# Kernel tuning notes

Hardware: AMD Instinct MI355X
Metric: run time of the kernel (lower is better)

## Reference

```python
import jax, jax.numpy as jnp
import numpy as np

COMMA_ID = 1010   # BERT wordpiece id for ','
H, NH, HD = 768, 8, 96
B, S = 64, 512
NSEG = 17         # 16 commas per row -> 17 segments
EPS = 1e-5


def setup_inputs() -> dict:
    key = jax.random.key(0)
    ks = jax.random.split(key, 16)
    text_hs = jax.random.normal(ks[0], (B, S, H), jnp.float32)
    cols_hs = jax.random.normal(ks[1], (B, S, H), jnp.float32)
    ids = jax.random.randint(ks[2], (B, S), 0, 30522)
    ids = jnp.where(ids == COMMA_ID, COMMA_ID + 1, ids)  # avoid accidental commas
    comma_pos = jnp.arange(16, 257, 16)                  # 16 commas per row
    ids = ids.at[:, comma_pos].set(COMMA_ID)
    sc = 0.02
    wq = jax.random.normal(ks[3], (H, H), jnp.float32) * sc
    wk = jax.random.normal(ks[4], (H, H), jnp.float32) * sc
    wv = jax.random.normal(ks[5], (H, H), jnp.float32) * sc
    bq = jnp.zeros((H,), jnp.float32)
    bk = jnp.zeros((H,), jnp.float32)
    bv = jnp.zeros((H,), jnp.float32)
    wo = jax.random.normal(ks[6], (H, H), jnp.float32) * sc
    bo = jnp.zeros((H,), jnp.float32)
    gamma = jnp.ones((H,), jnp.float32)
    beta = jnp.zeros((H,), jnp.float32)
    w_out = jax.random.normal(ks[7], (1, H), jnp.float32) * sc
    b_out = jnp.zeros((1,), jnp.float32)
    return dict(text_hs=text_hs, cols_hs=cols_hs, wq=wq, wk=wk, wv=wv,
                bq=bq, bk=bk, bv=bv, wo=wo, bo=bo, gamma=gamma, beta=beta,
                w_out=w_out, b_out=b_out, columns_input_ids=ids, n_segments=NSEG)


def _forward(text_hs, cols_hs, wq, wk, wv, bq, bk, bv, wo, bo,
             gamma, beta, w_out, b_out, columns_input_ids, n_segments):
    t = text_hs[:, 1:, :]   # drop first token, as in forward()  [B, L, H]
    c = cols_hs[:, 1:, :]
    L = t.shape[1]
    # --- nn.MultiheadAttention(query=cols, key=value=text), batch_first ---
    q = c @ wq.T + bq
    k = t @ wk.T + bk
    v = t @ wv.T + bv
    split = lambda x: x.reshape(x.shape[0], -1, NH, HD).transpose(0, 2, 1, 3)
    scores = jnp.einsum('bhqd,bhkd->bhqk', split(q), split(k)) / np.sqrt(HD).astype(np.float32)
    attn = jax.nn.softmax(scores, axis=-1)
    ctx = jnp.einsum('bhqk,bhkd->bhqd', attn, split(v))
    ctx = ctx.transpose(0, 2, 1, 3).reshape(c.shape[0], L, H)
    attn_out = ctx @ wo.T + bo
    # --- BatchNorm1d over channels (training-mode batch stats) ---
    xt = attn_out.transpose(0, 2, 1)            # [B, H, L]
    mu = xt.mean(axis=(0, 2), keepdims=True)
    var = xt.var(axis=(0, 2), keepdims=True)     # biased, as torch BN normalization
    xn = (xt - mu) / jnp.sqrt(var + EPS) * gamma[None, :, None] + beta[None, :, None]
    cross_out = c + xn.transpose(0, 2, 1)       # residual add
    fv = (cross_out @ w_out.T + b_out).squeeze(-1)   # [B, L] scores per token
    # --- compose_outputs: mean-pool comma-delimited ragged spans ---
    is_comma = columns_input_ids[:, :L] == COMMA_ID
    seg = jnp.cumsum(is_comma.astype(jnp.int32), axis=1) - is_comma.astype(jnp.int32)
    mask = (jnp.arange(L)[None, :] >= 1) & (~is_comma)    # slice_start=1, commas excluded
    oh = ((seg[:, :, None] == jnp.arange(n_segments)[None, None, :])
          & mask[:, :, None]).astype(fv.dtype)            # [B, L, J]
    sums = jnp.einsum('blj,bl->bj', oh, fv)
    cnt = oh.sum(axis=1)
    return sums / jnp.maximum(cnt, 1.0)                   # [B, n_segments]


def reference(text_hs, cols_hs, wq, wk, wv, bq, bk, bv, wo, bo,
              gamma, beta, w_out, b_out, columns_input_ids, n_segments):
    return _forward(text_hs, cols_hs, wq, wk, wv, bq, bk, bv, wo, bo,
                    gamma, beta, w_out, b_out, columns_input_ids, n_segments)
```

## Files before the change

### kernel.cpp

```cpp
#include <hip/hip_runtime.h>
#include <hip/hip_bf16.h>

#define COMMA_IDC 1010
#define NHEAD 8
#define Ll 511
#define Mrows 32704
#define NSEG 17

typedef __attribute__((ext_vector_type(8))) short bf16x8;
typedef __attribute__((ext_vector_type(4))) float f32x4;
typedef unsigned short u16;
typedef unsigned int u32;
typedef unsigned long long u64;

__device__ __forceinline__ u16 f2b(float f) {
  __hip_bfloat16 h = __float2bfloat16(f);
  return *reinterpret_cast<u16*>(&h);
}
__device__ __forceinline__ float b2f(u16 u) {
  u32 x = ((u32)u) << 16;
  return __builtin_bit_cast(float, x);
}

__device__ __forceinline__ void gld_lds16(const void* g, void* l) {
  __builtin_amdgcn_global_load_lds(
      (const __attribute__((address_space(1))) void*)(u64)g,
      (__attribute__((address_space(3))) void*)(u32)(u64)l,
      16, 0, 0);
}

#define MFMA16(a, b, c) __builtin_amdgcn_mfma_f32_16x16x32_bf16(a, b, c, 0, 0, 0)
#define LGKM0 do { asm volatile("s_waitcnt lgkmcnt(0)" ::: "memory"); __builtin_amdgcn_sched_barrier(0); } while (0)

__global__ void conv_w(const float4* __restrict__ wq, const float4* __restrict__ wk,
                       const float4* __restrict__ wv, const float4* __restrict__ wo,
                       ushort4* __restrict__ wqkvb, ushort4* __restrict__ wob) {
  int i = blockIdx.x * 256 + threadIdx.x;
  int seg = i / 147456, off = i - seg * 147456;
  const float4* s = (seg == 0) ? wq : ((seg == 1) ? wk : ((seg == 2) ? wv : wo));
  ushort4* d = (seg == 3) ? wob : (wqkvb + seg * 147456);
  float4 v = s[off];
  ushort4 o; o.x = f2b(v.x); o.y = f2b(v.y); o.z = f2b(v.z); o.w = f2b(v.w);
  d[off] = o;
}

__global__ void zero_kernel(float* p, int n) {
  int i = blockIdx.x * 256 + threadIdx.x;
  if (i < n) p[i] = 0.f;
}

#define LDA(db, i, kk) (*(const bf16x8*)(sMem + (db) + wr * 8192 + ((i) * 16 + fr) * 64 + ((((kk) * 4 + fq) ^ xm) << 3)))
#define LDW(db, j, kk) (*(const bf16x8*)(sMem + (db) + 16384 + (((wc * 64 + (j) * 16) >> 7) * 8192) + \
                     (((wc * 64 + (j) * 16) & 127) + fr) * 64 + ((((kk) * 4 + fq) ^ xm) << 3)))

template<int NTILES, int NOUT, int QNT, bool AF32, bool DO_STATS>
__global__ __launch_bounds__(512, 2) void gemm256(
    const void* __restrict__ A0v, const void* __restrict__ A1v, const u16* __restrict__ W,
    const float* __restrict__ b0, const float* __restrict__ b1, const float* __restrict__ b2,
    u16* __restrict__ outp, float* __restrict__ ssum, float* __restrict__ ssq)
{
  __shared__ __align__(16) u16 sMem[65536];
  const int tid = threadIdx.x;
  const int lane = tid & 63, wid = tid >> 6;
  const int fr = lane & 15, fq = lane >> 4;
  const int wr = wid >> 2, wc = wid & 3;
  const int xm = fr & 7;

  int fid = blockIdx.x;
  int xcd = fid & 7, w = fid >> 3;
  int mrow = xcd * 16 + w / NTILES;
  int ncol = w - (w / NTILES) * NTILES;
  const int m0 = mrow * 256, n0 = ncol * 256;

  const int rS = tid >> 3;
  const int cS = (tid & 7) ^ (rS & 7);
  const u16* gW0 = W + (u64)(n0 + rS) * 768 + cS * 8;
  const u16* gW1 = W + (u64)(n0 + 128 + rS) * 768 + cS * 8;
  const u32 st0 = tid * 8;

  const float* fA = (ncol < QNT) ? (const float*)A0v : (const float*)A1v;
  const u16*   uA = (ncol < QNT) ? (const u16*)A0v : (const u16*)A1v;
  const float* aSrc[4];
  u32 aDst[4];
  if constexpr (AF32) {
#pragma unroll
    for (int c4 = 0; c4 < 4; c4++) {
      int c = tid + c4 * 512;
      int half = c >> 10, rowin = (c >> 3) & 127, p = c & 7;
      int m = m0 + half * 128 + rowin;
      if (m > Mrows - 1) m = Mrows - 1;
      int srcrow = m + m / 511 + 1;
      int s = p ^ (rowin & 7);
      aSrc[c4] = fA + (u64)srcrow * 768 + s * 8;
      aDst[c4] = (u32)(half * 8192 + rowin * 64 + p * 8);
    }
  }
  const u16* gA0u = nullptr;
  const u16* gA1u = nullptr;
  if constexpr (!AF32) {
    gA0u = uA + (u64)(m0 + rS) * 768 + cS * 8;
    gA1u = uA + (u64)(m0 + 128 + rS) * 768 + cS * 8;
  }

  f32x4 acc[8][4] = {};
  bf16x8 af[4][2], wf[4][2];
  float4 rA[8];

  auto stageW = [&](int buf, int kt) {
    const int kb = kt * 64;
    const u32 db = (u32)buf * 32768 + 16384;
    gld_lds16(gW0 + kb, sMem + db + st0);
    gld_lds16(gW0 + kb + 49152, sMem + db + st0 + 4096);
    gld_lds16(gW1 + kb, sMem + db + 8192 + st0);
    gld_lds16(gW1 + kb + 49152, sMem + db + 8192 + st0 + 4096);
  };
  auto stageAu = [&](int buf, int kt) {
    const int kb = kt * 64;
    const u32 db = (u32)buf * 32768;
    gld_lds16(gA0u + kb, sMem + db + st0);
    gld_lds16(gA0u + kb + 49152, sMem + db + st0 + 4096);
    gld_lds16(gA1u + kb, sMem + db + 8192 + st0);
    gld_lds16(gA1u + kb + 49152, sMem + db + 8192 + st0 + 4096);
  };
  auto loadA = [&](int kt) {
#pragma unroll
    for (int c4 = 0; c4 < 4; c4++) {
      rA[2 * c4]     = *(const float4*)(aSrc[c4] + kt * 64);
      rA[2 * c4 + 1] = *(const float4*)(aSrc[c4] + kt * 64 + 4);
    }
  };
  auto writeA = [&](int buf) {
    const u32 db = (u32)buf * 32768;
#pragma unroll
    for (int c4 = 0; c4 < 4; c4++) {
      const float4 x = rA[2 * c4], y = rA[2 * c4 + 1];
      bf16x8 v;
      v[0] = (short)f2b(x.x); v[1] = (short)f2b(x.y); v[2] = (short)f2b(x.z); v[3] = (short)f2b(x.w);
      v[4] = (short)f2b(y.x); v[5] = (short)f2b(y.y); v[6] = (short)f2b(y.z); v[7] = (short)f2b(y.w);
      *(bf16x8*)(sMem + db + aDst[c4]) = v;
    }
  };

  if constexpr (AF32) {
    stageW(0, 0);
    loadA(0);
    writeA(0);
    loadA(1);
  } else {
    stageAu(0, 0);
    stageW(0, 0);
    asm volatile("s_waitcnt vmcnt(0)" ::: "memory");
  }
  LGKM0;
  __builtin_amdgcn_s_barrier();

  for (int kt = 0; kt < 12; ++kt) {
    const u32 db = (u32)(kt & 1) * 32768;
#pragma unroll
    for (int i = 0; i < 4; i++) { af[i][0] = LDA(db, i, 0); af[i][1] = LDA(db, i, 1); }
#pragma unroll
    for (int j = 0; j < 4; j++) { wf[j][0] = LDW(db, j, 0); wf[j][1] = LDW(db, j, 1); }
    if (kt + 1 < 12) {
      if constexpr (AF32) {
        writeA((kt + 1) & 1);
        stageW((kt + 1) & 1, kt + 1);
        if (kt + 2 < 12) loadA(kt + 2);
      } else {
        stageAu((kt + 1) & 1, kt + 1);
        stageW((kt + 1) & 1, kt + 1);
      }
    }
    __builtin_amdgcn_s_barrier();
    LGKM0;
    __builtin_amdgcn_s_setprio(1);
#pragma unroll
    for (int i = 0; i < 4; i++)
#pragma unroll
      for (int j = 0; j < 4; j++) {
        acc[i][j] = MFMA16(af[i][0], wf[j][0], acc[i][j]);
        acc[i][j] = MFMA16(af[i][1], wf[j][1], acc[i][j]);
      }
    __builtin_amdgcn_s_setprio(0);
    __builtin_amdgcn_s_barrier();
#pragma unroll
    for (int i = 0; i < 4; i++) { af[i][0] = LDA(db, i + 4, 0); af[i][1] = LDA(db, i + 4, 1); }
    LGKM0;
    __builtin_amdgcn_s_setprio(1);
#pragma unroll
    for (int i = 0; i < 4; i++)
#pragma unroll
      for (int j = 0; j < 4; j++) {
        acc[i + 4][j] = MFMA16(af[i][0], wf[j][0], acc[i + 4][j]);
        acc[i + 4][j] = MFMA16(af[i][1], wf[j][1], acc[i + 4][j]);
      }
    __builtin_amdgcn_s_setprio(0);
    if (kt + 1 < 12) {
      if constexpr (AF32) {
        if (kt + 2 < 12) { asm volatile("s_waitcnt vmcnt(8)" ::: "memory"); }
        else             { asm volatile("s_waitcnt vmcnt(0)" ::: "memory"); }
      } else {
        asm volatile("s_waitcnt vmcnt(0)" ::: "memory");
      }
    }
    __builtin_amdgcn_s_barrier();
  }

  const float* bp = (n0 < 768) ? b0 : ((n0 < 1536) ? b1 : b2);
  const int bcol = n0 % 768;
  float bj[4];
#pragma unroll
  for (int j = 0; j < 4; j++) bj[j] = bp[bcol + wc * 64 + j * 16 + fr];

  if constexpr (DO_STATS) {
#pragma unroll
    for (int j = 0; j < 4; j++) {
      float s = 0.f, q = 0.f;
#pragma unroll
      for (int i = 0; i < 8; i++)
#pragma unroll
        for (int r = 0; r < 4; r++) {
          int m = m0 + wr * 128 + i * 16 + fq * 4 + r;
          float v = acc[i][j][r] + bj[j];
          if (m < Mrows) { s += v; q += v * v; }
        }
      s += __shfl_xor(s, 16, 64); s += __shfl_xor(s, 32, 64);
      q += __shfl_xor(q, 16, 64); q += __shfl_xor(q, 32, 64);
      if (fq == 0) {
        int col = n0 + wc * 64 + j * 16 + fr;
        atomicAdd(&ssum[col], s);
        atomicAdd(&ssq[col], q);
      }
    }
  }

#pragma unroll
  for (int h = 0; h < 2; h++) {
    __syncthreads();
    if (wr == h) {
#pragma unroll
      for (int i = 0; i < 8; i++)
#pragma unroll
        for (int j = 0; j < 4; j++)
#pragma unroll
          for (int r = 0; r < 4; r++)
            sMem[(i * 16 + fq * 4 + r) * 264 + wc * 64 + j * 16 + fr] = f2b(acc[i][j][r] + bj[j]);
    }
    __syncthreads();
#pragma unroll
    for (int it = 0; it < 8; it++) {
      int chunk = tid + it * 512;
      int lr = chunk >> 5, ch = chunk & 31;
      *(bf16x8*)(outp + (u64)(m0 + h * 128 + lr) * NOUT + n0 + ch * 8) =
          *(const bf16x8*)(sMem + lr * 264 + ch * 8);
    }
  }
}

__global__ __launch_bounds__(256) void vtrans(const u16* __restrict__ QKV, u16* __restrict__ VT) {
  __shared__ __align__(16) u16 sT[128 * 128];
  int bh = blockIdx.y;
  int b = bh >> 3, h = bh & 7;
  int l0 = blockIdx.x * 128;
  u16* outp = VT + (u64)bh * 96 * 512;
  int t = threadIdx.x;
#pragma unroll
  for (int k = 0; k < 6; k++) {
    int c = t + k * 256;
    int l = c / 12, ch = c - l * 12;
    int lc = l0 + l; if (lc > 510) lc = 510;
    bf16x8 v = *(const bf16x8*)(QKV + (u64)(b * 511 + lc) * 2304 + 1536 + h * 96 + ch * 8);
    int chunk = l * 16 + (ch ^ ((l >> 3) & 7));
    *(bf16x8*)(sT + chunk * 8) = v;
  }
  __syncthreads();
#pragma unroll
  for (int k = 0; k < 6; k++) {
    int c = t + k * 256;
    int d = c >> 4, lch = c & 15;
    u16 vals[8];
#pragma unroll
    for (int k2 = 0; k2 < 8; k2++) {
      int r = lch * 8 + k2;
      int idx = r * 128 + (((d >> 3) ^ (lch & 7)) << 3) + (d & 7);
      vals[k2] = sT[idx];
    }
    bf16x8 o;
#pragma unroll
    for (int k2 = 0; k2 < 8; k2++) o[k2] = (short)vals[k2];
    *(bf16x8*)(outp + (u64)d * 512 + l0 + lch * 8) = o;
  }
}

#define PST 68
__global__ __launch_bounds__(256) void attn_kernel(
    const u16* __restrict__ QKV, const u16* __restrict__ VT, u16* __restrict__ ctxb)
{
  __shared__ __align__(16) u16 sK[64 * 96];
  __shared__ __align__(16) u16 sV[96 * 64];
  __shared__ __align__(16) u16 sP[4][16 * PST];
  const int tid = threadIdx.x, lane = tid & 63, wid = tid >> 6;
  int fid = blockIdx.x;
  int xcd = fid & 7, slot = (fid >> 3) & 3, grp = fid >> 5;
  int bh = grp * 8 + xcd;
  int b = bh >> 3, h = bh & 7;
  int q0 = slot * 128;
  const int fr = lane & 15, fq = lane >> 4;
  const u64 mb = (u64)(b * 511);
  const u64 hbV = (u64)bh * 96 * 512;

  bf16x8 qf[2][3];
#pragma unroll
  for (int sub = 0; sub < 2; sub++) {
    int qr = q0 + wid * 32 + sub * 16 + fr; if (qr > 510) qr = 510;
#pragma unroll
    for (int ks = 0; ks < 3; ks++)
      qf[sub][ks] = *(const bf16x8*)(QKV + (mb + qr) * 2304 + h * 96 + ks * 32 + fq * 8);
  }

  f32x4 ctx[2][6] = {};
  f32x4 sumP[2] = {};

  int kRow[3]; u32 kOffG[3], vOffG[3];
  u16 *kDst[3], *vDst[3];
#pragma unroll
  for (int k = 0; k < 3; k++) {
    int c = wid * 64 + lane + k * 256;
    int r = c / 12, p = c - r * 12;
    int s = p - (r % 12); if (s < 0) s += 12;
    kRow[k] = r;
    kOffG[k] = 768 + h * 96 + s * 8;
    kDst[k] = sK + (u32)(wid * 64 + k * 256) * 8;
    int d = c >> 3, pv = c & 7;
    int sv = pv ^ (d & 7);
    vOffG[k] = (u32)(d * 512 + sv * 8);
    vDst[k] = sV + (u32)(wid * 64 + k * 256) * 8;
  }

  const float cs = 0.10206207261596575f;
  u16* pw = &sP[wid][0];

  for (int kv0 = 0; kv0 < 511; kv0 += 64) {
    __syncthreads();
#pragma unroll
    for (int k = 0; k < 3; k++) {
      int row = kv0 + kRow[k]; if (row > 510) row = 510;
      gld_lds16(QKV + (mb + row) * 2304 + kOffG[k], kDst[k]);
    }
#pragma unroll
    for (int k = 0; k < 3; k++)
      gld_lds16(VT + hbV + vOffG[k] + kv0, vDst[k]);
    __syncthreads();

    bf16x8 kf[4][3];
#pragma unroll
    for (int kv16 = 0; kv16 < 4; kv16++) {
      int r = kv16 * 16 + fr;
      int rm = r % 12;
#pragma unroll
      for (int ks = 0; ks < 3; ks++) {
        int sidx = ks * 4 + fq + rm; if (sidx >= 12) sidx -= 12;
        kf[kv16][ks] = *(const bf16x8*)(sK + (r * 12 + sidx) * 8);
      }
    }

#pragma unroll
    for (int sub = 0; sub < 2; sub++) {
      f32x4 s[4] = {};
#pragma unroll
      for (int kv16 = 0; kv16 < 4; kv16++)
#pragma unroll
        for (int ks = 0; ks < 3; ks++)
          s[kv16] = MFMA16(qf[sub][ks], kf[kv16][ks], s[kv16]);

#pragma unroll
      for (int kv16 = 0; kv16 < 4; kv16++) {
        bool ok = (kv0 + kv16 * 16 + fr) < Ll;
#pragma unroll
        for (int r = 0; r < 4; r++) {
          float e = __expf(s[kv16][r] * cs);
          e = ok ? e : 0.f;
          sumP[sub][r] += e;
          pw[(fq * 4 + r) * PST + kv16 * 16 + fr] = f2b(e);
        }
      }
      bf16x8 pf0 = *(const bf16x8*)(pw + fr * PST + fq * 8);
      bf16x8 pf1 = *(const bf16x8*)(pw + fr * PST + 32 + fq * 8);
#pragma unroll
      for (int df = 0; df < 6; df++) {
        int row = df * 16 + fr;
        int xv = fr & 7;
        bf16x8 vf0 = *(const bf16x8*)(sV + row * 64 + ((fq ^ xv) << 3));
        bf16x8 vf1 = *(const bf16x8*)(sV + row * 64 + (((4 + fq) ^ xv) << 3));
        ctx[sub][df] = MFMA16(pf0, vf0, ctx[sub][df]);
        ctx[sub][df] = MFMA16(pf1, vf1, ctx[sub][df]);
      }
    }
  }

#pragma unroll
  for (int sub = 0; sub < 2; sub++) {
    float inv[4];
#pragma unroll
    for (int r = 0; r < 4; r++) {
      float s = sumP[sub][r];
      s += __shfl_xor(s, 1, 64);
      s += __shfl_xor(s, 2, 64);
      s += __shfl_xor(s, 4, 64);
      s += __shfl_xor(s, 8, 64);
      inv[r] = 1.f / s;
    }
#pragma unroll
    for (int df = 0; df < 6; df++) {
#pragma unroll
      for (int r = 0; r < 4; r++) {
        int q = q0 + wid * 32 + sub * 16 + fq * 4 + r;
        if (q < Ll)
          ctxb[(u64)(b * Ll + q) * 768 + h * 96 + df * 16 + fr] = f2b(ctx[sub][df][r] * inv[r]);
      }
    }
  }
}

__global__ __launch_bounds__(256) void derived_kernel(
    const float* __restrict__ ssum, const float* __restrict__ ssq,
    const float* __restrict__ w_out, const float* __restrict__ b_out,
    const float* __restrict__ gamma, const float* __restrict__ beta,
    float* __restrict__ weff, float* __restrict__ consts)
{
  __shared__ float red[256];
  int t = threadIdx.x;
  float acc = 0.f;
  const float invN = 1.f / 32704.f;
#pragma unroll
  for (int i = 0; i < 3; i++) {
    int hh = t + i * 256;
    float mu = ssum[hh] * invN;
    float var = ssq[hh] * invN - mu * mu;
    float rstd = 1.f / sqrtf(var + 1e-5f);
    float we = w_out[hh] * gamma[hh] * rstd;
    weff[hh] = we;
    acc += w_out[hh] * beta[hh] - we * mu;
  }
  red[t] = acc; __syncthreads();
  for (int s = 128; s > 0; s >>= 1) { if (t < s) red[t] += red[t + s]; __syncthreads(); }
  if (t == 0) consts[0] = b_out[0] + red[0];
}

__global__ __launch_bounds__(256) void fv_kernel(
    const u16* __restrict__ ao, const float* __restrict__ cols,
    const float* __restrict__ w_out, const float* __restrict__ weff,
    const float* __restrict__ consts, float* __restrict__ fv)
{
  int lane = threadIdx.x & 63, wid = threadIdx.x >> 6;
  int m = blockIdx.x * 4 + wid;
  if (m >= Mrows) return;
  int bidx = m / 511, l = m - bidx * 511;
  const u16* ap = ao + (u64)m * 768;
  const float* cp = cols + (u64)(bidx * 512 + l + 1) * 768;
  float acc = 0.f;
#pragma unroll
  for (int i = 0; i < 12; i++) {
    int hh = lane + i * 64;
    acc += b2f(ap[hh]) * weff[hh] + cp[hh] * w_out[hh];
  }
#pragma unroll
  for (int off = 1; off < 64; off <<= 1) acc += __shfl_xor(acc, off, 64);
  if (lane == 0) fv[m] = acc + consts[0];
}

__global__ __launch_bounds__(64) void seg_kernel(
    const float* __restrict__ fv, const int* __restrict__ ids, float* __restrict__ out)
{
  __shared__ float ssum[NSEG];
  __shared__ int scnt[NSEG];
  int lane = threadIdx.x;
  int b = blockIdx.x;
  if (lane < NSEG) { ssum[lane] = 0.f; scnt[lane] = 0; }
  __syncthreads();
  int carry = 0;
  for (int it = 0; it < 8; it++) {
    int l = it * 64 + lane;
    bool active = l < Ll;
    int id = active ? ids[b * 512 + l] : 0;
    bool comma = active && (id == COMMA_IDC);
    u64 cmask = __ballot(comma);
    int seg = carry + __popcll(cmask & ((1ull << lane) - 1ull));
    bool valid = active && (l >= 1) && !comma;
    if (valid && seg < NSEG) {
      atomicAdd(&ssum[seg], fv[b * Ll + l]);
      atomicAdd(&scnt[seg], 1);
    }
    carry += __popcll(cmask);
  }
  __syncthreads();
  if (lane < NSEG) {
    float c = (float)scnt[lane];
    out[b * NSEG + lane] = ssum[lane] / fmaxf(c, 1.f);
  }
}

extern "C" void kernel_launch(void* const* d_in, const int* in_sizes, int n_in,
                              void* d_out, int out_size, void* d_ws, size_t ws_size,
                              hipStream_t stream)
{
  const float* text  = (const float*)d_in[0];
  const float* cols  = (const float*)d_in[1];
  const float* wq    = (const float*)d_in[2];
  const float* wk    = (const float*)d_in[3];
  const float* wvp   = (const float*)d_in[4];
  const float* bq    = (const float*)d_in[5];
  const float* bk    = (const float*)d_in[6];
  const float* bv    = (const float*)d_in[7];
  const float* wo    = (const float*)d_in[8];
  const float* bo    = (const float*)d_in[9];
  const float* gamma = (const float*)d_in[10];
  const float* beta  = (const float*)d_in[11];
  const float* w_out = (const float*)d_in[12];
  const float* b_out = (const float*)d_in[13];
  const int*   ids   = (const int*)d_in[14];
  float* out = (float*)d_out;

  char* ws = (char*)d_ws;
  u16* VTb   = (u16*)(ws + 0ull);
  u16* wqkvb = (u16*)(ws + 50331648ull);
  u16* wob   = (u16*)(ws + 53870592ull);
  float* ssum   = (float*)(ws + 55050240ull);
  float* ssq    = ssum + 768;
  float* weff   = ssum + 1536;
  float* consts = ssum + 2304;
  float* fv     = (float*)(ws + 55050240ull + 16384ull);
  u16* QKVb  = (u16*)(ws + 56623104ull);
  u16* ctxb  = (u16*)(ws + 207618048ull);
  u16* aob   = QKVb;

  conv_w<<<2304, 256, 0, stream>>>(
      (const float4*)wq, (const float4*)wk, (const float4*)wvp, (const float4*)wo,
      (ushort4*)wqkvb, (ushort4*)wob);
  zero_kernel<<<6, 256, 0, stream>>>(ssum, 1536);

  gemm256<9, 2304, 3, true, false><<<1152, 512, 0, stream>>>(
      cols, text, wqkvb, bq, bk, bv, QKVb, nullptr, nullptr);
  vtrans<<<dim3(4, 512), 256, 0, stream>>>(QKVb, VTb);
  attn_kernel<<<2048, 256, 0, stream>>>(QKVb, VTb, ctxb);

  gemm256<3, 768, 99, false, true><<<384, 512, 0, stream>>>(
      ctxb, ctxb, wob, bo, bo, bo, aob, ssum, ssq);
  derived_kernel<<<1, 256, 0, stream>>>(ssum, ssq, w_out, b_out, gamma, beta, weff, consts);
  fv_kernel<<<8176, 256, 0, stream>>>(aob, cols, w_out, weff, consts, fv);
  seg_kernel<<<64, 64, 0, stream>>>(fv, ids, out);
}
```

Before: 462.5 us.

## Pre-convert activations to bf16 and restructure GEMM into four-phase pipelined quadrants

Adds a separate kernel that slices and converts the cols and text activations to bf16, so the QKV GEMM can stage A through direct global-to-LDS loads instead of converting fp32 in registers. The GEMM main loop is split into four sub-phases, each issuing one quarter of the next tile's loads interleaved with MFMA quadrants and fine-grained vmcnt waits. The warp-to-tile mapping is also changed to an interleaved layout. fv_kernel now reads the bf16 cols copy, which adds a full extra read and write pass over both inputs and slightly lowers the precision of the residual term.

```diff
diff --git a/kernel.cpp b/kernel.cpp
--- a/kernel.cpp
+++ b/kernel.cpp
@@ -31,6 +31,20 @@
 
 #define MFMA16(a, b, c) __builtin_amdgcn_mfma_f32_16x16x32_bf16(a, b, c, 0, 0, 0)
 #define LGKM0 do { asm volatile("s_waitcnt lgkmcnt(0)" ::: "memory"); __builtin_amdgcn_sched_barrier(0); } while (0)
+#define VMC(n) asm volatile("s_waitcnt vmcnt(" #n ")" ::: "memory")
+
+__global__ void conv_sliced2(const float4* __restrict__ s0, const float4* __restrict__ s1,
+                             ushort4* __restrict__ d0, ushort4* __restrict__ d1) {
+  const float4* src = blockIdx.z ? s1 : s0;
+  ushort4* dst = blockIdx.z ? d1 : d0;
+  int b = blockIdx.y;
+  int idx = blockIdx.x * 256 + threadIdx.x;
+  if (idx >= Ll * 192) return;
+  int l = idx / 192, c = idx - l * 192;
+  float4 v = src[(b * 512 + l + 1) * 192 + c];
+  ushort4 o; o.x = f2b(v.x); o.y = f2b(v.y); o.z = f2b(v.z); o.w = f2b(v.w);
+  dst[(b * Ll + l) * 192 + c] = o;
+}
 
 __global__ void conv_w(const float4* __restrict__ wq, const float4* __restrict__ wk,
                        const float4* __restrict__ wv, const float4* __restrict__ wo,
@@ -49,13 +63,12 @@
   if (i < n) p[i] = 0.f;
 }
 
-#define LDA(db, i, kk) (*(const bf16x8*)(sMem + (db) + wr * 8192 + ((i) * 16 + fr) * 64 + ((((kk) * 4 + fq) ^ xm) << 3)))
-#define LDW(db, j, kk) (*(const bf16x8*)(sMem + (db) + 16384 + (((wc * 64 + (j) * 16) >> 7) * 8192) + \
-                     (((wc * 64 + (j) * 16) & 127) + fr) * 64 + ((((kk) * 4 + fq) ^ xm) << 3)))
-
-template<int NTILES, int NOUT, int QNT, bool AF32, bool DO_STATS>
+#define LDA8(db, i, kk) (*(const bf16x8*)(sMem + (db) + ((i) * 32 + wr * 16 + fr) * 64 + ((((kk) * 4 + fq) ^ xm) << 3)))
+#define LDW8(db, j, kk) (*(const bf16x8*)(sMem + (db) + 16384 + ((j) * 64 + wc * 16 + fr) * 64 + ((((kk) * 4 + fq) ^ xm) << 3)))
+
+template<int NTILES, int NOUT, int QNT, bool DO_STATS>
 __global__ __launch_bounds__(512, 2) void gemm256(
-    const void* __restrict__ A0v, const void* __restrict__ A1v, const u16* __restrict__ W,
+    const u16* __restrict__ A0, const u16* __restrict__ A1, const u16* __restrict__ W,
     const float* __restrict__ b0, const float* __restrict__ b1, const float* __restrict__ b2,
     u16* __restrict__ outp, float* __restrict__ ssum, float* __restrict__ ssq)
 {
@@ -71,145 +84,171 @@
   int mrow = xcd * 16 + w / NTILES;
   int ncol = w - (w / NTILES) * NTILES;
   const int m0 = mrow * 256, n0 = ncol * 256;
+  const u16* __restrict__ A = (ncol < QNT) ? A0 : A1;
 
   const int rS = tid >> 3;
   const int cS = (tid & 7) ^ (rS & 7);
+  const u16* gA0 = A + (u64)(m0 + rS) * 768 + cS * 8;
   const u16* gW0 = W + (u64)(n0 + rS) * 768 + cS * 8;
-  const u16* gW1 = W + (u64)(n0 + 128 + rS) * 768 + cS * 8;
   const u32 st0 = tid * 8;
 
-  const float* fA = (ncol < QNT) ? (const float*)A0v : (const float*)A1v;
-  const u16*   uA = (ncol < QNT) ? (const u16*)A0v : (const u16*)A1v;
-  const float* aSrc[4];
-  u32 aDst[4];
-  if constexpr (AF32) {
-#pragma unroll
-    for (int c4 = 0; c4 < 4; c4++) {
-      int c = tid + c4 * 512;
-      int half = c >> 10, rowin = (c >> 3) & 127, p = c & 7;
-      int m = m0 + half * 128 + rowin;
-      if (m > Mrows - 1) m = Mrows - 1;
-      int srcrow = m + m / 511 + 1;
-      int s = p ^ (rowin & 7);
-      aSrc[c4] = fA + (u64)srcrow * 768 + s * 8;
-      aDst[c4] = (u32)(half * 8192 + rowin * 64 + p * 8);
-    }
-  }
-  const u16* gA0u = nullptr;
-  const u16* gA1u = nullptr;
-  if constexpr (!AF32) {
-    gA0u = uA + (u64)(m0 + rS) * 768 + cS * 8;
-    gA1u = uA + (u64)(m0 + 128 + rS) * 768 + cS * 8;
-  }
+  auto stALO = [&](u32 db, int kb) {
+    gld_lds16(gA0 + kb, sMem + db + st0);
+    gld_lds16(gA0 + kb + 49152, sMem + db + st0 + 4096);
+  };
+  auto stWLO = [&](u32 db, int kb) {
+    gld_lds16(gW0 + kb, sMem + db + 16384 + st0);
+    gld_lds16(gW0 + kb + 49152, sMem + db + 16384 + st0 + 4096);
+  };
+  auto stAHI = [&](u32 db, int kb) {
+    gld_lds16(gA0 + kb + 98304, sMem + db + 8192 + st0);
+    gld_lds16(gA0 + kb + 147456, sMem + db + 8192 + st0 + 4096);
+  };
+  auto stWHI = [&](u32 db, int kb) {
+    gld_lds16(gW0 + kb + 98304, sMem + db + 24576 + st0);
+    gld_lds16(gW0 + kb + 147456, sMem + db + 24576 + st0 + 4096);
+  };
 
   f32x4 acc[8][4] = {};
-  bf16x8 af[4][2], wf[4][2];
-  float4 rA[8];
-
-  auto stageW = [&](int buf, int kt) {
-    const int kb = kt * 64;
-    const u32 db = (u32)buf * 32768 + 16384;
-    gld_lds16(gW0 + kb, sMem + db + st0);
-    gld_lds16(gW0 + kb + 49152, sMem + db + st0 + 4096);
-    gld_lds16(gW1 + kb, sMem + db + 8192 + st0);
-    gld_lds16(gW1 + kb + 49152, sMem + db + 8192 + st0 + 4096);
-  };
-  auto stageAu = [&](int buf, int kt) {
-    const int kb = kt * 64;
-    const u32 db = (u32)buf * 32768;
-    gld_lds16(gA0u + kb, sMem + db + st0);
-    gld_lds16(gA0u + kb + 49152, sMem + db + st0 + 4096);
-    gld_lds16(gA1u + kb, sMem + db + 8192 + st0);
-    gld_lds16(gA1u + kb + 49152, sMem + db + 8192 + st0 + 4096);
-  };
-  auto loadA = [&](int kt) {
-#pragma unroll
-    for (int c4 = 0; c4 < 4; c4++) {
-      rA[2 * c4]     = *(const float4*)(aSrc[c4] + kt * 64);
-      rA[2 * c4 + 1] = *(const float4*)(aSrc[c4] + kt * 64 + 4);
-    }
-  };
-  auto writeA = [&](int buf) {
-    const u32 db = (u32)buf * 32768;
-#pragma unroll
-    for (int c4 = 0; c4 < 4; c4++) {
-      const float4 x = rA[2 * c4], y = rA[2 * c4 + 1];
-      bf16x8 v;
-      v[0] = (short)f2b(x.x); v[1] = (short)f2b(x.y); v[2] = (short)f2b(x.z); v[3] = (short)f2b(x.w);
-      v[4] = (short)f2b(y.x); v[5] = (short)f2b(y.y); v[6] = (short)f2b(y.z); v[7] = (short)f2b(y.w);
-      *(bf16x8*)(sMem + db + aDst[c4]) = v;
-    }
-  };
-
-  if constexpr (AF32) {
-    stageW(0, 0);
-    loadA(0);
-    writeA(0);
-    loadA(1);
-  } else {
-    stageAu(0, 0);
-    stageW(0, 0);
-    asm volatile("s_waitcnt vmcnt(0)" ::: "memory");
-  }
-  LGKM0;
+  bf16x8 af[4][2], wl[2][2], wh[2][2];
+
+  stALO(0, 0); stWLO(0, 0); stAHI(0, 0); stWHI(0, 0);
+  VMC(4);
   __builtin_amdgcn_s_barrier();
 
-  for (int kt = 0; kt < 12; ++kt) {
+#pragma unroll 1
+  for (int kt = 0; kt < 11; ++kt) {
     const u32 db = (u32)(kt & 1) * 32768;
-#pragma unroll
-    for (int i = 0; i < 4; i++) { af[i][0] = LDA(db, i, 0); af[i][1] = LDA(db, i, 1); }
-#pragma unroll
-    for (int j = 0; j < 4; j++) { wf[j][0] = LDW(db, j, 0); wf[j][1] = LDW(db, j, 1); }
-    if (kt + 1 < 12) {
-      if constexpr (AF32) {
-        writeA((kt + 1) & 1);
-        stageW((kt + 1) & 1, kt + 1);
-        if (kt + 2 < 12) loadA(kt + 2);
-      } else {
-        stageAu((kt + 1) & 1, kt + 1);
-        stageW((kt + 1) & 1, kt + 1);
-      }
-    }
+    const u32 nb = db ^ 32768u;
+    const int kb1 = (kt + 1) * 64;
+
+#pragma unroll
+    for (int i = 0; i < 4; i++) { af[i][0] = LDA8(db, i, 0); af[i][1] = LDA8(db, i, 1); }
+#pragma unroll
+    for (int j = 0; j < 2; j++) { wl[j][0] = LDW8(db, j, 0); wl[j][1] = LDW8(db, j, 1); }
+    stALO(nb, kb1);
     __builtin_amdgcn_s_barrier();
     LGKM0;
     __builtin_amdgcn_s_setprio(1);
 #pragma unroll
     for (int i = 0; i < 4; i++)
 #pragma unroll
-      for (int j = 0; j < 4; j++) {
-        acc[i][j] = MFMA16(af[i][0], wf[j][0], acc[i][j]);
-        acc[i][j] = MFMA16(af[i][1], wf[j][1], acc[i][j]);
+      for (int j = 0; j < 2; j++) {
+        acc[i][j] = MFMA16(af[i][0], wl[j][0], acc[i][j]);
+        acc[i][j] = MFMA16(af[i][1], wl[j][1], acc[i][j]);
       }
     __builtin_amdgcn_s_setprio(0);
-    __builtin_amdgcn_s_barrier();
-#pragma unroll
-    for (int i = 0; i < 4; i++) { af[i][0] = LDA(db, i + 4, 0); af[i][1] = LDA(db, i + 4, 1); }
+    VMC(4);
+    __builtin_amdgcn_s_barrier();
+
+#pragma unroll
+    for (int i = 0; i < 4; i++) { af[i][0] = LDA8(db, i + 4, 0); af[i][1] = LDA8(db, i + 4, 1); }
+    stWLO(nb, kb1);
+    __builtin_amdgcn_s_barrier();
     LGKM0;
     __builtin_amdgcn_s_setprio(1);
 #pragma unroll
     for (int i = 0; i < 4; i++)
 #pragma unroll
-      for (int j = 0; j < 4; j++) {
-        acc[i + 4][j] = MFMA16(af[i][0], wf[j][0], acc[i + 4][j]);
-        acc[i + 4][j] = MFMA16(af[i][1], wf[j][1], acc[i + 4][j]);
+      for (int j = 0; j < 2; j++) {
+        acc[i + 4][j] = MFMA16(af[i][0], wl[j][0], acc[i + 4][j]);
+        acc[i + 4][j] = MFMA16(af[i][1], wl[j][1], acc[i + 4][j]);
       }
     __builtin_amdgcn_s_setprio(0);
-    if (kt + 1 < 12) {
-      if constexpr (AF32) {
-        if (kt + 2 < 12) { asm volatile("s_waitcnt vmcnt(8)" ::: "memory"); }
-        else             { asm volatile("s_waitcnt vmcnt(0)" ::: "memory"); }
-      } else {
-        asm volatile("s_waitcnt vmcnt(0)" ::: "memory");
-      }
-    }
-    __builtin_amdgcn_s_barrier();
+    VMC(4);
+    __builtin_amdgcn_s_barrier();
+
+#pragma unroll
+    for (int j = 0; j < 2; j++) { wh[j][0] = LDW8(db, j + 2, 0); wh[j][1] = LDW8(db, j + 2, 1); }
+    stAHI(nb, kb1);
+    __builtin_amdgcn_s_barrier();
+    LGKM0;
+    __builtin_amdgcn_s_setprio(1);
+#pragma unroll
+    for (int i = 0; i < 4; i++)
+#pragma unroll
+      for (int j = 0; j < 2; j++) {
+        acc[i + 4][j + 2] = MFMA16(af[i][0], wh[j][0], acc[i + 4][j + 2]);
+        acc[i + 4][j + 2] = MFMA16(af[i][1], wh[j][1], acc[i + 4][j + 2]);
+      }
+    __builtin_amdgcn_s_setprio(0);
+    __builtin_amdgcn_s_barrier();
+
+#pragma unroll
+    for (int i = 0; i < 4; i++) { af[i][0] = LDA8(db, i, 0); af[i][1] = LDA8(db, i, 1); }
+    stWHI(nb, kb1);
+    __builtin_amdgcn_s_barrier();
+    LGKM0;
+    __builtin_amdgcn_s_setprio(1);
+#pragma unroll
+    for (int i = 0; i < 4; i++)
+#pragma unroll
+      for (int j = 0; j < 2; j++) {
+        acc[i][j + 2] = MFMA16(af[i][0], wh[j][0], acc[i][j + 2]);
+        acc[i][j + 2] = MFMA16(af[i][1], wh[j][1], acc[i][j + 2]);
+      }
+    __builtin_amdgcn_s_setprio(0);
+    VMC(4);
+    __builtin_amdgcn_s_barrier();
+  }
+
+  {
+    const u32 db = 32768u;
+#pragma unroll
+    for (int i = 0; i < 4; i++) { af[i][0] = LDA8(db, i, 0); af[i][1] = LDA8(db, i, 1); }
+#pragma unroll
+    for (int j = 0; j < 2; j++) { wl[j][0] = LDW8(db, j, 0); wl[j][1] = LDW8(db, j, 1); }
+    __builtin_amdgcn_s_barrier();
+    LGKM0;
+#pragma unroll
+    for (int i = 0; i < 4; i++)
+#pragma unroll
+      for (int j = 0; j < 2; j++) {
+        acc[i][j] = MFMA16(af[i][0], wl[j][0], acc[i][j]);
+        acc[i][j] = MFMA16(af[i][1], wl[j][1], acc[i][j]);
+      }
+    VMC(2);
+    __builtin_amdgcn_s_barrier();
+#pragma unroll
+    for (int i = 0; i < 4; i++) { af[i][0] = LDA8(db, i + 4, 0); af[i][1] = LDA8(db, i + 4, 1); }
+    __builtin_amdgcn_s_barrier();
+    LGKM0;
+#pragma unroll
+    for (int i = 0; i < 4; i++)
+#pragma unroll
+      for (int j = 0; j < 2; j++) {
+        acc[i + 4][j] = MFMA16(af[i][0], wl[j][0], acc[i + 4][j]);
+        acc[i + 4][j] = MFMA16(af[i][1], wl[j][1], acc[i + 4][j]);
+      }
+    VMC(0);
+    __builtin_amdgcn_s_barrier();
+#pragma unroll
+    for (int j = 0; j < 2; j++) { wh[j][0] = LDW8(db, j + 2, 0); wh[j][1] = LDW8(db, j + 2, 1); }
+    LGKM0;
+#pragma unroll
+    for (int i = 0; i < 4; i++)
+#pragma unroll
+      for (int j = 0; j < 2; j++) {
+        acc[i + 4][j + 2] = MFMA16(af[i][0], wh[j][0], acc[i + 4][j + 2]);
+        acc[i + 4][j + 2] = MFMA16(af[i][1], wh[j][1], acc[i + 4][j + 2]);
+      }
+#pragma unroll
+    for (int i = 0; i < 4; i++) { af[i][0] = LDA8(db, i, 0); af[i][1] = LDA8(db, i, 1); }
+    LGKM0;
+#pragma unroll
+    for (int i = 0; i < 4; i++)
+#pragma unroll
+      for (int j = 0; j < 2; j++) {
+        acc[i][j + 2] = MFMA16(af[i][0], wh[j][0], acc[i][j + 2]);
+        acc[i][j + 2] = MFMA16(af[i][1], wh[j][1], acc[i][j + 2]);
+      }
   }
 
   const float* bp = (n0 < 768) ? b0 : ((n0 < 1536) ? b1 : b2);
   const int bcol = n0 % 768;
   float bj[4];
 #pragma unroll
-  for (int j = 0; j < 4; j++) bj[j] = bp[bcol + wc * 64 + j * 16 + fr];
+  for (int j = 0; j < 4; j++) bj[j] = bp[bcol + j * 64 + wc * 16 + fr];
 
   if constexpr (DO_STATS) {
 #pragma unroll
@@ -219,14 +258,14 @@
       for (int i = 0; i < 8; i++)
 #pragma unroll
         for (int r = 0; r < 4; r++) {
-          int m = m0 + wr * 128 + i * 16 + fq * 4 + r;
+          int m = m0 + i * 32 + wr * 16 + fq * 4 + r;
           float v = acc[i][j][r] + bj[j];
           if (m < Mrows) { s += v; q += v * v; }
         }
       s += __shfl_xor(s, 16, 64); s += __shfl_xor(s, 32, 64);
       q += __shfl_xor(q, 16, 64); q += __shfl_xor(q, 32, 64);
       if (fq == 0) {
-        int col = n0 + wc * 64 + j * 16 + fr;
+        int col = n0 + j * 64 + wc * 16 + fr;
         atomicAdd(&ssum[col], s);
         atomicAdd(&ssq[col], q);
       }
@@ -236,14 +275,15 @@
 #pragma unroll
   for (int h = 0; h < 2; h++) {
     __syncthreads();
-    if (wr == h) {
-#pragma unroll
-      for (int i = 0; i < 8; i++)
-#pragma unroll
-        for (int j = 0; j < 4; j++)
-#pragma unroll
-          for (int r = 0; r < 4; r++)
-            sMem[(i * 16 + fq * 4 + r) * 264 + wc * 64 + j * 16 + fr] = f2b(acc[i][j][r] + bj[j]);
+#pragma unroll
+    for (int i2 = 0; i2 < 4; i2++) {
+      int i = h * 4 + i2;
+#pragma unroll
+      for (int j = 0; j < 4; j++)
+#pragma unroll
+        for (int r = 0; r < 4; r++)
+          sMem[(i2 * 32 + wr * 16 + fq * 4 + r) * 264 + j * 64 + wc * 16 + fr] =
+              f2b(acc[i][j][r] + bj[j]);
     }
     __syncthreads();
 #pragma unroll
@@ -447,21 +487,20 @@
 }
 
 __global__ __launch_bounds__(256) void fv_kernel(
-    const u16* __restrict__ ao, const float* __restrict__ cols,
+    const u16* __restrict__ ao, const u16* __restrict__ cb,
     const float* __restrict__ w_out, const float* __restrict__ weff,
     const float* __restrict__ consts, float* __restrict__ fv)
 {
   int lane = threadIdx.x & 63, wid = threadIdx.x >> 6;
   int m = blockIdx.x * 4 + wid;
   if (m >= Mrows) return;
-  int bidx = m / 511, l = m - bidx * 511;
   const u16* ap = ao + (u64)m * 768;
-  const float* cp = cols + (u64)(bidx * 512 + l + 1) * 768;
+  const u16* cp = cb + (u64)m * 768;
   float acc = 0.f;
 #pragma unroll
   for (int i = 0; i < 12; i++) {
     int hh = lane + i * 64;
-    acc += b2f(ap[hh]) * weff[hh] + cp[hh] * w_out[hh];
+    acc += b2f(ap[hh]) * weff[hh] + b2f(cp[hh]) * w_out[hh];
   }
 #pragma unroll
   for (int off = 1; off < 64; off <<= 1) acc += __shfl_xor(acc, off, 64);
@@ -521,31 +560,35 @@
   float* out = (float*)d_out;
 
   char* ws = (char*)d_ws;
-  u16* VTb   = (u16*)(ws + 0ull);
-  u16* wqkvb = (u16*)(ws + 50331648ull);
-  u16* wob   = (u16*)(ws + 53870592ull);
-  float* ssum   = (float*)(ws + 55050240ull);
+  u16* cb    = (u16*)(ws + 0ull);
+  u16* tb    = (u16*)(ws + 50331648ull);
+  u16* wqkvb = (u16*)(ws + 100663296ull);
+  u16* wob   = (u16*)(ws + 104202240ull);
+  u16* QKVb  = (u16*)(ws + 105381888ull);
+  u16* ctxb  = (u16*)(ws + 256376832ull);
+  u16* VTb   = tb;
+  u16* aob   = QKVb;
+  float* ssum   = (float*)(ws + 105381888ull + 50331648ull);
   float* ssq    = ssum + 768;
   float* weff   = ssum + 1536;
   float* consts = ssum + 2304;
-  float* fv     = (float*)(ws + 55050240ull + 16384ull);
-  u16* QKVb  = (u16*)(ws + 56623104ull);
-  u16* ctxb  = (u16*)(ws + 207618048ull);
-  u16* aob   = QKVb;
-
+  float* fv     = (float*)((char*)ssum + 16384ull);
+
+  conv_sliced2<<<dim3(384, 64, 2), 256, 0, stream>>>(
+      (const float4*)cols, (const float4*)text, (ushort4*)cb, (ushort4*)tb);
   conv_w<<<2304, 256, 0, stream>>>(
       (const float4*)wq, (const float4*)wk, (const float4*)wvp, (const float4*)wo,
       (ushort4*)wqkvb, (ushort4*)wob);
-  zero_kernel<<<6, 256, 0, stream>>>(ssum, 1536);
-
-  gemm256<9, 2304, 3, true, false><<<1152, 512, 0, stream>>>(
-      cols, text, wqkvb, bq, bk, bv, QKVb, nullptr, nullptr);
+
+  gemm256<9, 2304, 3, false><<<1152, 512, 0, stream>>>(
+      cb, tb, wqkvb, bq, bk, bv, QKVb, nullptr, nullptr);
   vtrans<<<dim3(4, 512), 256, 0, stream>>>(QKVb, VTb);
   attn_kernel<<<2048, 256, 0, stream>>>(QKVb, VTb, ctxb);
 
-  gemm256<3, 768, 99, false, true><<<384, 512, 0, stream>>>(
+  zero_kernel<<<6, 256, 0, stream>>>(ssum, 1536);
+  gemm256<3, 768, 99, true><<<384, 512, 0, stream>>>(
       ctxb, ctxb, wob, bo, bo, bo, aob, ssum, ssq);
   derived_kernel<<<1, 256, 0, stream>>>(ssum, ssq, w_out, b_out, gamma, beta, weff, consts);
-  fv_kernel<<<8176, 256, 0, stream>>>(aob, cols, w_out, weff, consts, fv);
+  fv_kernel<<<8176, 256, 0, stream>>>(aob, cb, w_out, weff, consts, fv);
   seg_kernel<<<64, 64, 0, stream>>>(fv, ids, out);
 }
```

Result: faster. 412.7 us (-10.8%).
